# Optimization experiments

Measured on AMD Instinct MI355X. Metric: run time of the kernel, lower is better.

## Reference

```python
import jax, jax.numpy as jnp
import numpy as np
from jax import lax

L = 8
PATCH = 3
DIRS = [(0, 1), (1, 0), (1, 1), (1, -1)]


def _pair_indices():
    coords = np.arange(PATCH * PATCH)
    rr, cc = coords // PATCH, coords % PATCH
    i1s, i2s = [], []
    for dr, dc in DIRS:
        m = (rr + dr >= 0) & (rr + dr < PATCH) & (cc + dc >= 0) & (cc + dc < PATCH)
        i1s.append(coords[m])
        i2s.append((rr[m] + dr) * PATCH + (cc[m] + dc))
    return np.concatenate(i1s), np.concatenate(i2s)

_I1, _I2 = _pair_indices()


def conv_bn_silu(x, w, s, b, pad):
    # Conv2d(bias=False) + eval-mode BatchNorm folded into (s, b) + SiLU
    y = lax.conv_general_dilated(x, w, (1, 1), [(pad, pad), (pad, pad)],
                                 dimension_numbers=("NCHW", "OIHW", "NCHW"))
    y = y * s[None, :, None, None] + b[None, :, None, None]
    return jax.nn.silu(y)


def glcm_feats(x):
    B, C, H, W = x.shape
    pad = PATCH // 2
    xp = jnp.pad(x, ((0, 0), (0, 0), (pad, pad), (pad, pad)), mode="edge")
    # unfold: (B, C, 9, H, W)
    patches = jnp.stack([xp[:, :, i:i + H, j:j + W]
                         for i in range(PATCH) for j in range(PATCH)], axis=2)
    q = jnp.clip((patches * (L - 1)).astype(jnp.int32), 0, L - 1)
    q = q.reshape(B * C, PATCH * PATCH, H * W)
    # co-occurrence pair indices for all 4 directions, concatenated: (BC, K, HW)
    idx = q[:, _I1, :] * L + q[:, _I2, :]
    idx = idx.transpose(0, 2, 1)  # (BC, HW, K)
    # per-pixel local histogram over L*L bins (scatter-add)
    hist = jax.vmap(jax.vmap(
        lambda v: jnp.zeros((L * L,), x.dtype).at[v].add(1.0)))(idx)
    hist = hist / len(DIRS)  # reduce_mode='average'
    s = jnp.maximum(hist.sum(-1, keepdims=True), 1e-6)
    p = hist / s  # (BC, HW, L*L)
    li = jnp.arange(L, dtype=x.dtype)
    diff = li[:, None] - li[None, :]
    diff_sq = (diff ** 2).reshape(-1)
    abs_d = jnp.abs(diff).reshape(-1)
    contrast = (p * diff_sq).sum(-1)
    energy = (p * p).sum(-1)
    entropy = -(p * jnp.log(p + 1e-6)).sum(-1)
    homog = (p / (1.0 + abs_d)).sum(-1)
    f = jnp.stack([contrast, energy, entropy, homog], axis=-1)  # (BC, HW, 4)
    f = f.reshape(B, C, H * W, 4).mean(axis=1)  # average over channels
    return f.transpose(0, 2, 1).reshape(B, 4, H, W)


def setup_inputs() -> dict:
    key = jax.random.key(0)
    B, C, H, W = 4, 64, 80, 80
    c_, cb, c2 = 32, 16, 64
    ks = iter(jax.random.split(key, 20))
    x = jax.random.uniform(next(ks), (B, C, H, W), jnp.float32)

    def conv_p(cin, cout, ksz):
        w = jax.random.normal(next(ks), (cout, cin, ksz, ksz), jnp.float32) / np.sqrt(cin * ksz * ksz)
        s = jax.random.uniform(next(ks), (cout,), jnp.float32, 0.5, 1.5)
        b = jax.random.normal(next(ks), (cout,), jnp.float32) * 0.1
        return w, s, b

    cv1_w, cv1_s, cv1_b = conv_p(C + 4, c_, 1)
    cv2_w, cv2_s, cv2_b = conv_p(C + 4, c_, 1)
    m1_w, m1_s, m1_b = conv_p(c_, cb, 1)
    m2_w, m2_s, m2_b = conv_p(cb, c_, 3)
    cv3_w, cv3_s, cv3_b = conv_p(2 * c_, c2, 1)
    return dict(x=x, cv1_w=cv1_w, cv1_s=cv1_s, cv1_b=cv1_b,
                cv2_w=cv2_w, cv2_s=cv2_s, cv2_b=cv2_b,
                m1_w=m1_w, m1_s=m1_s, m1_b=m1_b,
                m2_w=m2_w, m2_s=m2_s, m2_b=m2_b,
                cv3_w=cv3_w, cv3_s=cv3_s, cv3_b=cv3_b)


def reference(x, cv1_w, cv1_s, cv1_b, cv2_w, cv2_s, cv2_b,
              m1_w, m1_s, m1_b, m2_w, m2_s, m2_b,
              cv3_w, cv3_s, cv3_b):
    g = glcm_feats(x)
    xc = jnp.concatenate([x, g], axis=1)  # (B, C+4, H, W)
    a = conv_bn_silu(xc, cv1_w, cv1_s, cv1_b, 0)
    y = conv_bn_silu(a, m1_w, m1_s, m1_b, 0)
    y = conv_bn_silu(y, m2_w, m2_s, m2_b, 1)
    a = a + y  # Bottleneck shortcut (c1 == c2)
    b = conv_bn_silu(xc, cv2_w, cv2_s, cv2_b, 0)
    return conv_bn_silu(jnp.concatenate([a, b], axis=1), cv3_w, cv3_s, cv3_b, 0)
```

## Files before the change

### kernel.cpp

```cpp
#include <hip/hip_runtime.h>
#include <math.h>

constexpr int B = 4, C = 64, H = 80, W = 80;
constexpr int HW = H * W;
constexpr int NPIX = B * HW;
constexpr int PXB = 16;

typedef unsigned u32;

static __device__ __forceinline__ float silu(float v) {
    float e = __expf(-v);
    return v * __builtin_amdgcn_rcpf(1.0f + e);
}

static __device__ __forceinline__ u32 pks(u32 a, u32 b){u32 d; asm("v_pk_sub_u16 %0,%1,%2":"=v"(d):"v"(a),"v"(b)); return d;}
static __device__ __forceinline__ u32 pka(u32 a, u32 b){u32 d; asm("v_pk_add_u16 %0,%1,%2":"=v"(d):"v"(a),"v"(b)); return d;}
static __device__ __forceinline__ u32 pkm(u32 a, u32 b){u32 d; asm("v_pk_mul_lo_u16 %0,%1,%2":"=v"(d):"v"(a),"v"(b)); return d;}
static __device__ __forceinline__ u32 pkmin(u32 a, u32 b){u32 d; asm("v_pk_min_u16 %0,%1,%2":"=v"(d):"v"(a),"v"(b)); return d;}
static __device__ __forceinline__ u32 pkmaxi(u32 a, u32 b){u32 d; asm("v_pk_max_i16 %0,%1,%2":"=v"(d):"v"(a),"v"(b)); return d;}
static __device__ __forceinline__ float cb0(u32 a){float f; asm("v_cvt_f32_ubyte0 %0,%1":"=v"(f):"v"(a)); return f;}
static __device__ __forceinline__ float cb2(u32 a){float f; asm("v_cvt_f32_ubyte2 %0,%1":"=v"(f):"v"(a)); return f;}

static __device__ __forceinline__ u32 permb(u32 hi, u32 lo, u32 sel){
    u32 d; asm("v_perm_b32 %0, %1, %2, %3" : "=v"(d) : "v"(hi), "v"(lo), "v"(sel)); return d;}
static __device__ __forceinline__ u32 sad8(u32 a, u32 b, u32 c){
    u32 d; asm("v_sad_u8 %0, %1, %2, %3" : "=v"(d) : "v"(a), "v"(b), "v"(c)); return d;}

static __device__ __forceinline__ void ce(u32 &x, u32 &y) {
    u32 mn, mx;
    asm("v_pk_min_u16 %0, %2, %3\n\t"
        "v_pk_max_u16 %1, %2, %3"
        : "=&v"(mn), "=v"(mx) : "v"(x), "v"(y));
    x = mn; y = mx;
}

__global__ __launch_bounds__(512, 4) void glcm_stage1_kernel(
    const float* __restrict__ x,
    const float* __restrict__ w1, const float* __restrict__ s1, const float* __restrict__ b1,
    const float* __restrict__ w2, const float* __restrict__ s2, const float* __restrict__ b2,
    const float* __restrict__ wm1, const float* __restrict__ sm1, const float* __restrict__ bm1,
    float* __restrict__ a, float* __restrict__ bbuf, float* __restrict__ y16) {
    __shared__ u32 qcell[32][3][18];
    __shared__ __align__(16) float xs[PXB][72];
    __shared__ __align__(16) float ws1[32][68];
    __shared__ __align__(16) float ws2[32][68];
    __shared__ __align__(16) float wsm1[16][32];
    __shared__ float aT[PXB][33];
    __shared__ float red[8][PXB][4];

    const int t = threadIdx.x;
    const int p0g = blockIdx.x * PXB;
    const int bb  = p0g / HW;
    const int hw0 = p0g - bb * HW;
    const int h0  = hw0 / W;
    const int c0g = hw0 - h0 * W;

    {
        const float4* w1f = (const float4*)w1;
        const float4* w2f = (const float4*)w2;
        float4* s1f = (float4*)&ws1[0][0];
        float4* s2f = (float4*)&ws2[0][0];
        for (int e = t; e < 544; e += 512) { s1f[e] = w1f[e]; s2f[e] = w2f[e]; }
        if (t < 128) ((float4*)&wsm1[0][0])[t] = ((const float4*)wm1)[t];
    }
    for (int e = t; e < 32 * 3 * 18; e += 512) {
        const int grp = e / 54;
        const int rem = e - grp * 54;
        const int row = rem / 18;
        const int col = rem - row * 18;
        int gr = h0 + row - 1;  gr = gr < 0 ? 0 : (gr > H - 1 ? H - 1 : gr);
        int gc = c0g + col - 1; gc = gc < 0 ? 0 : (gc > W - 1 ? W - 1 : gc);
        const float v0 = x[((size_t)(bb * C + grp * 2)) * HW + gr * W + gc];
        const float v1 = x[((size_t)(bb * C + grp * 2 + 1)) * HW + gr * W + gc];
        int q0 = (int)(v0 * 7.0f); q0 = q0 < 0 ? 0 : (q0 > 7 ? 7 : q0);
        int q1 = (int)(v1 * 7.0f); q1 = q1 < 0 ? 0 : (q1 > 7 ? 7 : q1);
        qcell[grp][row][col] = (u32)q0 | ((u32)q1 << 16);
        if (row == 1 && col >= 1 && col <= 16) {
            xs[col - 1][grp * 2]     = v0;
            xs[col - 1][grp * 2 + 1] = v1;
        }
    }
    __syncthreads();

    const int pxl = t & 15;
    const int grp = t >> 4;
    u32 qpk[9];
    #pragma unroll
    for (int r = 0; r < 3; ++r)
        #pragma unroll
        for (int k = 0; k < 3; ++k)
            qpk[r * 3 + k] = qcell[grp][r][pxl + k];

    static constexpr int PA[20] = {0,1,3,4,6,7, 0,1,2,3,4,5, 0,1,3,4, 1,2,4,5};
    static constexpr int PB[20] = {1,2,4,5,7,8, 3,4,5,6,7,8, 4,5,7,8, 3,4,6,7};

    const u32 ONEpk = 0x00010001u, EIGHTpk = 0x00080008u;
    u32 key[20];
    u32 csI = 0, hloI = 0, hhiI = 0;
    const u32 z0 = 0;
    #pragma unroll
    for (int j = 0; j < 10; ++j) {
        u32 adp0, adp1;
        {
            const u32 qa = qpk[PA[2*j]], qb = qpk[PB[2*j]];
            const u32 d = pks(qa, qb);
            adp0 = pkmaxi(d, pks(0u, d));
            key[2*j] = pka(pkm(qa, EIGHTpk), qb);
        }
        {
            const u32 qa = qpk[PA[2*j+1]], qb = qpk[PB[2*j+1]];
            const u32 d = pks(qa, qb);
            adp1 = pkmaxi(d, pks(0u, d));
            key[2*j+1] = pka(pkm(qa, EIGHTpk), qb);
        }
        const u32 pk4 = permb(adp1, adp0, 0x06040200u);
        csI  = sad8(permb(0x31241910u, 0x09040100u, pk4), z0, csI);
        hloI = sad8(permb(0x69788CA8u, 0xD218A448u, pk4), z0, hloI);
        hhiI = sad8(permb(0x00000000u, 0x00010103u, pk4), z0, hhiI);
    }

    #pragma unroll
    for (int p = 1; p < 32; p <<= 1) {
        #pragma unroll
        for (int k = p; k >= 1; k >>= 1) {
            const int jm = k % p;
            #pragma unroll
            for (int lo = 0; lo < 20; ++lo) {
                const int hi = lo + k;
                if (hi < 20 && lo >= jm && ((lo - jm) % (2 * k)) < k &&
                    (lo / (2 * p)) == (hi / (2 * p))) {
                    ce(key[lo], key[hi]);
                }
            }
        }
    }

    u32 eq[20];
    #pragma unroll
    for (int ai = 1; ai < 20; ++ai)
        eq[ai] = pks(ONEpk, pkmin(pks(key[ai], key[ai - 1]), ONEpk));

    u32 pc = 0, ps = 0, pv[20];
    pv[0] = 0;
    #pragma unroll
    for (int ai = 1; ai < 20; ++ai) {
        pc = pkm(pka(pc, ONEpk), eq[ai]);
        pv[ai] = pc;
        ps = pka(ps, pc);
    }
    float pr0, pr1;
    {
        const u32 m = pka(pv[19], ONEpk);
        pr0 = cb0(m); pr1 = cb2(m);
    }
    u32 rc = 0;
    #pragma unroll
    for (int ai = 18; ai >= 0; --ai) {
        rc = pkm(pka(rc, ONEpk), eq[ai + 1]);
        const u32 m = pka(pka(pv[ai], rc), ONEpk);
        pr0 *= cb0(m); pr1 *= cb2(m);
    }

    const int psum = (int)(ps & 0xFFFFu) + (int)(ps >> 16);
    const float lsum = __logf(pr0) + __logf(pr1);

    float fc = (float)csI * (1.f / 20.f);
    float fe = ((float)psum * 2.f + 40.f) * (1.f / 400.f);
    float fn = -(lsum + 40.f * -2.9957322736f) * (1.f / 20.f);
    float fh = (float)(hloI + (hhiI << 8)) * (1.f / 16800.f);

    fc += __shfl_xor(fc, 16); fe += __shfl_xor(fe, 16);
    fn += __shfl_xor(fn, 16); fh += __shfl_xor(fh, 16);
    fc += __shfl_xor(fc, 32); fe += __shfl_xor(fe, 32);
    fn += __shfl_xor(fn, 32); fh += __shfl_xor(fh, 32);
    const int wv = t >> 6;
    if ((t & 63) < 16) {
        red[wv][pxl][0] = fc; red[wv][pxl][1] = fe;
        red[wv][pxl][2] = fn; red[wv][pxl][3] = fh;
    }
    __syncthreads();
    if (t < 64) {
        const int p2 = t >> 2, f = t & 3;
        float s = 0.f;
        #pragma unroll
        for (int wq = 0; wq < 8; ++wq) s += red[wq][p2][f];
        xs[p2][64 + f] = s * (1.f / 64.f);
    }
    __syncthreads();

    {
        const int px = t & 15;
        const int oc = t >> 4;
        float acc1 = 0.f, acc2 = 0.f;
        #pragma unroll
        for (int k = 0; k < 17; ++k) {
            const float4 xv = *reinterpret_cast<const float4*>(&xs[px][k * 4]);
            const float4 wa = *reinterpret_cast<const float4*>(&ws1[oc][k * 4]);
            const float4 wb = *reinterpret_cast<const float4*>(&ws2[oc][k * 4]);
            acc1 += xv.x * wa.x + xv.y * wa.y + xv.z * wa.z + xv.w * wa.w;
            acc2 += xv.x * wb.x + xv.y * wb.y + xv.z * wb.z + xv.w * wb.w;
        }
        const int hw2 = hw0 + px;
        const float v1 = silu(acc1 * s1[oc] + b1[oc]);
        a[((size_t)(bb * 32 + oc)) * HW + hw2] = v1;
        aT[px][oc] = v1;
        bbuf[((size_t)(bb * 32 + oc)) * HW + hw2] = silu(acc2 * s2[oc] + b2[oc]);
    }
    __syncthreads();

    if (t < 256) {
        const int px = t & 15;
        const int oc = t >> 4;
        float acc = 0.f;
        #pragma unroll 8
        for (int ic = 0; ic < 32; ++ic)
            acc += aT[px][ic] * wsm1[oc][ic];
        y16[((size_t)(bb * 16 + oc)) * HW + hw0 + px] = silu(acc * sm1[oc] + bm1[oc]);
    }
}

__global__ __launch_bounds__(512) void m2cv3_kernel(
    const float* __restrict__ y16, const float* __restrict__ a,
    const float* __restrict__ bbuf,
    const float* __restrict__ wm2, const float* __restrict__ sm2, const float* __restrict__ bm2,
    const float* __restrict__ wc, const float* __restrict__ sc, const float* __restrict__ bc,
    float* __restrict__ out) {
    __shared__ float ys[16][4][82];
    __shared__ float a2[32][64];
    __shared__ float bs[32][64];
    const int t = threadIdx.x;
    const int p0 = blockIdx.x * 64;
    const int bi = p0 / HW;
    const int hw0 = p0 - bi * HW;
    const int h0 = hw0 / W;

    const float* yb = y16 + (size_t)(bi * 16) * HW;
    for (int e = t; e < 16 * 4 * 82; e += 512) {
        const int ch = e / 328;
        const int rem = e - ch * 328;
        const int row = rem / 82;
        const int col = rem - row * 82;
        const int r = h0 - 1 + row;
        const int c = col - 1;
        float v = 0.f;
        if ((unsigned)r < (unsigned)H && (unsigned)c < (unsigned)W)
            v = yb[(size_t)ch * HW + r * W + c];
        ys[ch][row][col] = v;
    }
    for (int e = t; e < 32 * 64; e += 512) {
        const int ic = e >> 6, px = e & 63;
        bs[ic][px] = bbuf[((size_t)(bi * 32 + ic)) * HW + hw0 + px];
    }
    __syncthreads();

    const int lane = t & 63;
    const int wv = __builtin_amdgcn_readfirstlane(t >> 6);
    const int hw = hw0 + lane;
    const int h = hw / W;
    const int w = hw - h * W;
    const int lr = h - h0;
    const int oc0 = wv * 4;

    float acc[4] = {0.f, 0.f, 0.f, 0.f};
    #pragma unroll 2
    for (int ic = 0; ic < 16; ++ic) {
        #pragma unroll
        for (int ky = 0; ky < 3; ++ky) {
            #pragma unroll
            for (int kx = 0; kx < 3; ++kx) {
                const float v = ys[ic][lr + ky][w + kx];
                const int tap = ic * 9 + ky * 3 + kx;
                #pragma unroll
                for (int j = 0; j < 4; ++j)
                    acc[j] += v * wm2[(oc0 + j) * 144 + tap];
            }
        }
    }
    #pragma unroll
    for (int j = 0; j < 4; ++j) {
        const int oc = oc0 + j;
        a2[oc][lane] = a[((size_t)(bi * 32 + oc)) * HW + hw]
                     + silu(acc[j] * sm2[oc] + bm2[oc]);
    }
    __syncthreads();
    const int oc3 = wv * 8;
    float c_[8] = {0.f, 0.f, 0.f, 0.f, 0.f, 0.f, 0.f, 0.f};
    #pragma unroll 4
    for (int ic = 0; ic < 32; ++ic) {
        const float av = a2[ic][lane];
        const float bv = bs[ic][lane];
        #pragma unroll
        for (int j = 0; j < 8; ++j) {
            c_[j] += av * wc[(oc3 + j) * 64 + ic];
            c_[j] += bv * wc[(oc3 + j) * 64 + 32 + ic];
        }
    }
    #pragma unroll
    for (int j = 0; j < 8; ++j) {
        const int oc = oc3 + j;
        out[((size_t)(bi * 64 + oc)) * HW + hw] = silu(c_[j] * sc[oc] + bc[oc]);
    }
}

extern "C" void kernel_launch(void* const* d_in, const int* in_sizes, int n_in,
                              void* d_out, int out_size, void* d_ws, size_t ws_size,
                              hipStream_t stream) {
    const float* x    = (const float*)d_in[0];
    const float* cv1w = (const float*)d_in[1];
    const float* cv1s = (const float*)d_in[2];
    const float* cv1b = (const float*)d_in[3];
    const float* cv2w = (const float*)d_in[4];
    const float* cv2s = (const float*)d_in[5];
    const float* cv2b = (const float*)d_in[6];
    const float* m1w  = (const float*)d_in[7];
    const float* m1s  = (const float*)d_in[8];
    const float* m1b  = (const float*)d_in[9];
    const float* m2w  = (const float*)d_in[10];
    const float* m2s  = (const float*)d_in[11];
    const float* m2b  = (const float*)d_in[12];
    const float* cv3w = (const float*)d_in[13];
    const float* cv3s = (const float*)d_in[14];
    const float* cv3b = (const float*)d_in[15];

    float* ws   = (float*)d_ws;
    float* a    = ws;
    float* bbuf = ws + 819200;
    float* y16  = ws + 1638400;

    glcm_stage1_kernel<<<NPIX / PXB, 512, 0, stream>>>(
        x, cv1w, cv1s, cv1b, cv2w, cv2s, cv2b, m1w, m1s, m1b, a, bbuf, y16);
    m2cv3_kernel<<<NPIX / 64, 512, 0, stream>>>(y16, a, bbuf, m2w, m2s, m2b,
                                                cv3w, cv3s, cv3b, (float*)d_out);
}
```

Before: 58.47 us.

## Fuse both stages into one persistent cooperative kernel with a grid barrier

```diff
diff --git a/kernel.cpp b/kernel.cpp
--- a/kernel.cpp
+++ b/kernel.cpp
@@ -1,10 +1,15 @@
 #include <hip/hip_runtime.h>
+#include <hip/hip_cooperative_groups.h>
 #include <math.h>
+
+namespace cg = cooperative_groups;
 
 constexpr int B = 4, C = 64, H = 80, W = 80;
 constexpr int HW = H * W;
 constexpr int NPIX = B * HW;
 constexpr int PXB = 16;
+constexpr int NTILE1 = NPIX / PXB;
+constexpr int NTILE2 = NPIX / 64;
 
 typedef unsigned u32;
 
@@ -34,35 +39,35 @@
     x = mn; y = mx;
 }
 
-__global__ __launch_bounds__(512, 4) void glcm_stage1_kernel(
+struct SmA {
+    u32   qcell[32][3][18];
+    float xs[PXB][76] __attribute__((aligned(16)));
+    float ws1[32][68] __attribute__((aligned(16)));
+    float ws2[32][68] __attribute__((aligned(16)));
+    float wsm1[16][32] __attribute__((aligned(16)));
+    float aT[PXB][33];
+    float red[8][PXB][4];
+};
+struct SmB {
+    float ys[16][4][82];
+    float a2[32][64];
+    float bs[32][64];
+};
+union SmemU { SmA a; SmB b; };
+
+static __device__ __forceinline__ void stage1_tile(
+    SmA& sm, int t, int tile,
     const float* __restrict__ x,
-    const float* __restrict__ w1, const float* __restrict__ s1, const float* __restrict__ b1,
-    const float* __restrict__ w2, const float* __restrict__ s2, const float* __restrict__ b2,
-    const float* __restrict__ wm1, const float* __restrict__ sm1, const float* __restrict__ bm1,
+    const float* __restrict__ s1, const float* __restrict__ b1,
+    const float* __restrict__ s2, const float* __restrict__ b2,
+    const float* __restrict__ sm1, const float* __restrict__ bm1,
     float* __restrict__ a, float* __restrict__ bbuf, float* __restrict__ y16) {
-    __shared__ u32 qcell[32][3][18];
-    __shared__ __align__(16) float xs[PXB][72];
-    __shared__ __align__(16) float ws1[32][68];
-    __shared__ __align__(16) float ws2[32][68];
-    __shared__ __align__(16) float wsm1[16][32];
-    __shared__ float aT[PXB][33];
-    __shared__ float red[8][PXB][4];
-
-    const int t = threadIdx.x;
-    const int p0g = blockIdx.x * PXB;
+    const int p0g = tile * PXB;
     const int bb  = p0g / HW;
     const int hw0 = p0g - bb * HW;
     const int h0  = hw0 / W;
     const int c0g = hw0 - h0 * W;
 
-    {
-        const float4* w1f = (const float4*)w1;
-        const float4* w2f = (const float4*)w2;
-        float4* s1f = (float4*)&ws1[0][0];
-        float4* s2f = (float4*)&ws2[0][0];
-        for (int e = t; e < 544; e += 512) { s1f[e] = w1f[e]; s2f[e] = w2f[e]; }
-        if (t < 128) ((float4*)&wsm1[0][0])[t] = ((const float4*)wm1)[t];
-    }
     for (int e = t; e < 32 * 3 * 18; e += 512) {
         const int grp = e / 54;
         const int rem = e - grp * 54;
@@ -74,10 +79,10 @@
         const float v1 = x[((size_t)(bb * C + grp * 2 + 1)) * HW + gr * W + gc];
         int q0 = (int)(v0 * 7.0f); q0 = q0 < 0 ? 0 : (q0 > 7 ? 7 : q0);
         int q1 = (int)(v1 * 7.0f); q1 = q1 < 0 ? 0 : (q1 > 7 ? 7 : q1);
-        qcell[grp][row][col] = (u32)q0 | ((u32)q1 << 16);
+        sm.qcell[grp][row][col] = (u32)q0 | ((u32)q1 << 16);
         if (row == 1 && col >= 1 && col <= 16) {
-            xs[col - 1][grp * 2]     = v0;
-            xs[col - 1][grp * 2 + 1] = v1;
+            sm.xs[col - 1][grp * 2]     = v0;
+            sm.xs[col - 1][grp * 2 + 1] = v1;
         }
     }
     __syncthreads();
@@ -89,7 +94,7 @@
     for (int r = 0; r < 3; ++r)
         #pragma unroll
         for (int k = 0; k < 3; ++k)
-            qpk[r * 3 + k] = qcell[grp][r][pxl + k];
+            qpk[r * 3 + k] = sm.qcell[grp][r][pxl + k];
 
     static constexpr int PA[20] = {0,1,3,4,6,7, 0,1,2,3,4,5, 0,1,3,4, 1,2,4,5};
     static constexpr int PB[20] = {1,2,4,5,7,8, 3,4,5,6,7,8, 4,5,7,8, 3,4,6,7};
@@ -175,16 +180,16 @@
     fn += __shfl_xor(fn, 32); fh += __shfl_xor(fh, 32);
     const int wv = t >> 6;
     if ((t & 63) < 16) {
-        red[wv][pxl][0] = fc; red[wv][pxl][1] = fe;
-        red[wv][pxl][2] = fn; red[wv][pxl][3] = fh;
+        sm.red[wv][pxl][0] = fc; sm.red[wv][pxl][1] = fe;
+        sm.red[wv][pxl][2] = fn; sm.red[wv][pxl][3] = fh;
     }
     __syncthreads();
     if (t < 64) {
         const int p2 = t >> 2, f = t & 3;
         float s = 0.f;
         #pragma unroll
-        for (int wq = 0; wq < 8; ++wq) s += red[wq][p2][f];
-        xs[p2][64 + f] = s * (1.f / 64.f);
+        for (int wq = 0; wq < 8; ++wq) s += sm.red[wq][p2][f];
+        sm.xs[p2][64 + f] = s * (1.f / 64.f);
     }
     __syncthreads();
 
@@ -194,16 +199,16 @@
         float acc1 = 0.f, acc2 = 0.f;
         #pragma unroll
         for (int k = 0; k < 17; ++k) {
-            const float4 xv = *reinterpret_cast<const float4*>(&xs[px][k * 4]);
-            const float4 wa = *reinterpret_cast<const float4*>(&ws1[oc][k * 4]);
-            const float4 wb = *reinterpret_cast<const float4*>(&ws2[oc][k * 4]);
+            const float4 xv = *reinterpret_cast<const float4*>(&sm.xs[px][k * 4]);
+            const float4 wa = *reinterpret_cast<const float4*>(&sm.ws1[oc][k * 4]);
+            const float4 wb = *reinterpret_cast<const float4*>(&sm.ws2[oc][k * 4]);
             acc1 += xv.x * wa.x + xv.y * wa.y + xv.z * wa.z + xv.w * wa.w;
             acc2 += xv.x * wb.x + xv.y * wb.y + xv.z * wb.z + xv.w * wb.w;
         }
         const int hw2 = hw0 + px;
         const float v1 = silu(acc1 * s1[oc] + b1[oc]);
         a[((size_t)(bb * 32 + oc)) * HW + hw2] = v1;
-        aT[px][oc] = v1;
+        sm.aT[px][oc] = v1;
         bbuf[((size_t)(bb * 32 + oc)) * HW + hw2] = silu(acc2 * s2[oc] + b2[oc]);
     }
     __syncthreads();
@@ -214,22 +219,31 @@
         float acc = 0.f;
         #pragma unroll 8
         for (int ic = 0; ic < 32; ++ic)
-            acc += aT[px][ic] * wsm1[oc][ic];
+            acc += sm.aT[px][ic] * sm.wsm1[oc][ic];
         y16[((size_t)(bb * 16 + oc)) * HW + hw0 + px] = silu(acc * sm1[oc] + bm1[oc]);
     }
 }
 
-__global__ __launch_bounds__(512) void m2cv3_kernel(
+static __device__ __forceinline__ void stage_weights(
+    SmA& sm, int t,
+    const float* __restrict__ w1, const float* __restrict__ w2,
+    const float* __restrict__ wm1) {
+    const float4* w1f = (const float4*)w1;
+    const float4* w2f = (const float4*)w2;
+    float4* s1f = (float4*)&sm.ws1[0][0];
+    float4* s2f = (float4*)&sm.ws2[0][0];
+    for (int e = t; e < 544; e += 512) { s1f[e] = w1f[e]; s2f[e] = w2f[e]; }
+    if (t < 128) ((float4*)&sm.wsm1[0][0])[t] = ((const float4*)wm1)[t];
+}
+
+static __device__ __forceinline__ void m2cv3_tile(
+    SmB& sm, int t, int tile,
     const float* __restrict__ y16, const float* __restrict__ a,
     const float* __restrict__ bbuf,
     const float* __restrict__ wm2, const float* __restrict__ sm2, const float* __restrict__ bm2,
     const float* __restrict__ wc, const float* __restrict__ sc, const float* __restrict__ bc,
     float* __restrict__ out) {
-    __shared__ float ys[16][4][82];
-    __shared__ float a2[32][64];
-    __shared__ float bs[32][64];
-    const int t = threadIdx.x;
-    const int p0 = blockIdx.x * 64;
+    const int p0 = tile * 64;
     const int bi = p0 / HW;
     const int hw0 = p0 - bi * HW;
     const int h0 = hw0 / W;
@@ -245,11 +259,11 @@
         float v = 0.f;
         if ((unsigned)r < (unsigned)H && (unsigned)c < (unsigned)W)
             v = yb[(size_t)ch * HW + r * W + c];
-        ys[ch][row][col] = v;
+        sm.ys[ch][row][col] = v;
     }
     for (int e = t; e < 32 * 64; e += 512) {
         const int ic = e >> 6, px = e & 63;
-        bs[ic][px] = bbuf[((size_t)(bi * 32 + ic)) * HW + hw0 + px];
+        sm.bs[ic][px] = bbuf[((size_t)(bi * 32 + ic)) * HW + hw0 + px];
     }
     __syncthreads();
 
@@ -268,7 +282,7 @@
         for (int ky = 0; ky < 3; ++ky) {
             #pragma unroll
             for (int kx = 0; kx < 3; ++kx) {
-                const float v = ys[ic][lr + ky][w + kx];
+                const float v = sm.ys[ic][lr + ky][w + kx];
                 const int tap = ic * 9 + ky * 3 + kx;
                 #pragma unroll
                 for (int j = 0; j < 4; ++j)
@@ -279,16 +293,16 @@
     #pragma unroll
     for (int j = 0; j < 4; ++j) {
         const int oc = oc0 + j;
-        a2[oc][lane] = a[((size_t)(bi * 32 + oc)) * HW + hw]
-                     + silu(acc[j] * sm2[oc] + bm2[oc]);
+        sm.a2[oc][lane] = a[((size_t)(bi * 32 + oc)) * HW + hw]
+                        + silu(acc[j] * sm2[oc] + bm2[oc]);
     }
     __syncthreads();
     const int oc3 = wv * 8;
     float c_[8] = {0.f, 0.f, 0.f, 0.f, 0.f, 0.f, 0.f, 0.f};
     #pragma unroll 4
     for (int ic = 0; ic < 32; ++ic) {
-        const float av = a2[ic][lane];
-        const float bv = bs[ic][lane];
+        const float av = sm.a2[ic][lane];
+        const float bv = sm.bs[ic][lane];
         #pragma unroll
         for (int j = 0; j < 8; ++j) {
             c_[j] += av * wc[(oc3 + j) * 64 + ic];
@@ -300,6 +314,55 @@
         const int oc = oc3 + j;
         out[((size_t)(bi * 64 + oc)) * HW + hw] = silu(c_[j] * sc[oc] + bc[oc]);
     }
+}
+
+__global__ __launch_bounds__(512, 4) void fused_kernel(
+    const float* __restrict__ x,
+    const float* __restrict__ w1, const float* __restrict__ s1, const float* __restrict__ b1,
+    const float* __restrict__ w2, const float* __restrict__ s2, const float* __restrict__ b2,
+    const float* __restrict__ wm1, const float* __restrict__ sm1, const float* __restrict__ bm1,
+    const float* __restrict__ wm2, const float* __restrict__ sm2, const float* __restrict__ bm2,
+    const float* __restrict__ wc, const float* __restrict__ sc, const float* __restrict__ bc,
+    float* __restrict__ a, float* __restrict__ bbuf, float* __restrict__ y16,
+    float* __restrict__ out) {
+    __shared__ SmemU sm;
+    const int t = threadIdx.x;
+
+    stage_weights(sm.a, t, w1, w2, wm1);
+    for (int tile = blockIdx.x; tile < NTILE1; tile += gridDim.x) {
+        __syncthreads();
+        stage1_tile(sm.a, t, tile, x, s1, b1, s2, b2, sm1, bm1, a, bbuf, y16);
+    }
+
+    cg::this_grid().sync();
+
+    for (int tile = blockIdx.x; tile < NTILE2; tile += gridDim.x) {
+        __syncthreads();
+        m2cv3_tile(sm.b, t, tile, y16, a, bbuf, wm2, sm2, bm2, wc, sc, bc, out);
+    }
+}
+
+__global__ __launch_bounds__(512, 4) void stage1_kernel(
+    const float* __restrict__ x,
+    const float* __restrict__ w1, const float* __restrict__ s1, const float* __restrict__ b1,
+    const float* __restrict__ w2, const float* __restrict__ s2, const float* __restrict__ b2,
+    const float* __restrict__ wm1, const float* __restrict__ sm1, const float* __restrict__ bm1,
+    float* __restrict__ a, float* __restrict__ bbuf, float* __restrict__ y16) {
+    __shared__ SmA sm;
+    const int t = threadIdx.x;
+    stage_weights(sm, t, w1, w2, wm1);
+    stage1_tile(sm, t, blockIdx.x, x, s1, b1, s2, b2, sm1, bm1, a, bbuf, y16);
+}
+
+__global__ __launch_bounds__(512, 4) void m2cv3_kernel(
+    const float* __restrict__ y16, const float* __restrict__ a,
+    const float* __restrict__ bbuf,
+    const float* __restrict__ wm2, const float* __restrict__ sm2, const float* __restrict__ bm2,
+    const float* __restrict__ wc, const float* __restrict__ sc, const float* __restrict__ bc,
+    float* __restrict__ out) {
+    __shared__ SmB sm;
+    m2cv3_tile(sm, threadIdx.x, blockIdx.x, y16, a, bbuf, wm2, sm2, bm2,
+               wc, sc, bc, out);
 }
 
 extern "C" void kernel_launch(void* const* d_in, const int* in_sizes, int n_in,
@@ -326,9 +389,33 @@
     float* a    = ws;
     float* bbuf = ws + 819200;
     float* y16  = ws + 1638400;
-
-    glcm_stage1_kernel<<<NPIX / PXB, 512, 0, stream>>>(
-        x, cv1w, cv1s, cv1b, cv2w, cv2s, cv2b, m1w, m1s, m1b, a, bbuf, y16);
-    m2cv3_kernel<<<NPIX / 64, 512, 0, stream>>>(y16, a, bbuf, m2w, m2s, m2b,
-                                                cv3w, cv3s, cv3b, (float*)d_out);
-}
+    float* outp = (float*)d_out;
+
+    void* args[] = {
+        (void*)&x,
+        (void*)&cv1w, (void*)&cv1s, (void*)&cv1b,
+        (void*)&cv2w, (void*)&cv2s, (void*)&cv2b,
+        (void*)&m1w,  (void*)&m1s,  (void*)&m1b,
+        (void*)&m2w,  (void*)&m2s,  (void*)&m2b,
+        (void*)&cv3w, (void*)&cv3s, (void*)&cv3b,
+        (void*)&a, (void*)&bbuf, (void*)&y16, (void*)&outp,
+    };
+
+    bool done = false;
+    int maxBlk = 0;
+    hipError_t qe = hipOccupancyMaxActiveBlocksPerMultiprocessor(
+        &maxBlk, (const void*)fused_kernel, 512, 0);
+    if (qe == hipSuccess && maxBlk > 0) {
+        int grid = maxBlk * 256;
+        if (grid > NTILE1) grid = NTILE1;
+        hipError_t le = hipLaunchCooperativeKernel(
+            (void*)fused_kernel, dim3(grid), dim3(512), args, 0, stream);
+        done = (le == hipSuccess);
+    }
+    if (!done) {
+        stage1_kernel<<<NTILE1, 512, 0, stream>>>(
+            x, cv1w, cv1s, cv1b, cv2w, cv2s, cv2b, m1w, m1s, m1b, a, bbuf, y16);
+        m2cv3_kernel<<<NTILE2, 512, 0, stream>>>(
+            y16, a, bbuf, m2w, m2s, m2b, cv3w, cv3s, cv3b, outp);
+    }
+}
```

After: 124.4 us. 2.13x slower.
